# Performance work log

Hardware: AMD Instinct MI355X
Metric: run time of the kernel (lower is better)

Reference implementation:

```python
import jax, jax.numpy as jnp
import numpy as np

DILATED = (1, 2, 3)
NUM_PROTOS = 100
PROTO_SIZE = 4
ENC_SIZE = 1600
NUM_CLASSES = 2
B, L = 64, 256

# num_filters split exactly as in torch: floor(P/len) each, first gets remainder
_nf = [NUM_PROTOS // len(DILATED)] * len(DILATED)
_nf[0] += NUM_PROTOS % len(DILATED)
NUM_FILTERS = tuple(_nf)  # (34, 33, 33)


def setup_inputs() -> dict:
    key = jax.random.key(0)
    k1, k2, k3 = jax.random.split(key, 3)
    embedding = jax.random.normal(k1, (B, L, ENC_SIZE), dtype=jnp.float32)
    # nn.init.uniform_ default is U[0,1)
    protolayer = jax.random.uniform(k2, (NUM_PROTOS, ENC_SIZE, PROTO_SIZE), dtype=jnp.float32)
    fc_w = jax.random.normal(k3, (NUM_CLASSES, NUM_PROTOS), dtype=jnp.float32) * 0.1
    return {"embedding": embedding, "protolayer": protolayer, "fc_w": fc_w}


def _l2_convolution(x_bel, protolayer):
    # x_bel: [B, L, E] -> [B, E, L] for NCH conv layout
    x = jnp.transpose(x_bel, (0, 2, 1))
    # sliding-window sum of x^2 computed ONCE per dilation (shared across protos,
    # mathematically identical to conv1d with all-ones weight)
    s = jnp.sum(x * x, axis=1)  # [B, L]
    p2_sum = jnp.sum(protolayer * protolayer, axis=(1, 2))  # [P]
    distances = []
    j = 0
    Lx = x.shape[2]
    for d, n in zip(DILATED, NUM_FILTERS):
        L_out = Lx - (PROTO_SIZE - 1) * d
        # windowed sum over K=PROTO_SIZE taps with dilation d: [B, L_out]
        x2_patch = sum(s[:, k * d:k * d + L_out] for k in range(PROTO_SIZE))
        # dilated cross-correlation x * p : [B, n, L_out]
        xp = jax.lax.conv_general_dilated(
            x, protolayer[j:j + n],
            window_strides=(1,), padding='VALID', rhs_dilation=(d,),
            dimension_numbers=('NCH', 'OIH', 'NCH'))
        dist = jnp.sqrt(jnp.abs(x2_patch[:, None, :] - 2.0 * xp
                                + p2_sum[j:j + n][None, :, None]))
        distances.append(dist)
        j += n
    return distances


def reference(embedding, protolayer, fc_w):
    distances = _l2_convolution(embedding, protolayer)
    prototype_distances = jnp.concatenate(
        [jnp.min(d, axis=2) for d in distances], axis=1)  # [B, P]
    class_out = prototype_distances @ fc_w.T  # [B, num_classes]
    return (prototype_distances, distances[0], distances[1], distances[2], class_out)
```

## Files before the change

kernel.cpp:

```cpp
#include <hip/hip_runtime.h>

#define B_   64
#define L_   256
#define E_   1600
#define P_   100
#define KP   4
#define N0 34
#define N1 33
#define N2 33
#define LOUT0 253
#define LOUT1 250
#define LOUT2 247
#define OFF_PD 0
#define OFF_D0 6400
#define OFF_D1 (OFF_D0 + B_*N0*LOUT0)
#define OFF_D2 (OFF_D1 + B_*N1*LOUT1)
#define OFF_CO (OFF_D2 + B_*N2*LOUT2)

#define WS_ABF  0ull
#define WS_BT   52428800ull
#define WS_S    (WS_BT + 1280000ull)
#define WS_P2   (WS_S + 65536ull)
#define WS_NEED (WS_P2 + 512ull)

#define TMF  96
#define BKB  128
#define BOFF2 12288

typedef float f32x4 __attribute__((ext_vector_type(4)));
typedef unsigned short ushort8v __attribute__((ext_vector_type(8)));
typedef __bf16 bf16x8 __attribute__((ext_vector_type(8)));
typedef _Float16 f16;

__device__ __forceinline__ unsigned short bf16rne(float f) {
    unsigned u = __float_as_uint(f);
    u += 0x7FFFu + ((u >> 16) & 1u);
    return (unsigned short)(u >> 16);
}

typedef __attribute__((address_space(3))) void lds_void_t;
typedef __attribute__((address_space(1))) void glb_void_t;

__device__ __forceinline__ void gload16(const void* g, void* l) {
    __builtin_amdgcn_global_load_lds((const glb_void_t*)g, (lds_void_t*)l, 16, 0, 0);
}


__global__ __launch_bounds__(256) void proto_prep_fast(
        const float* __restrict__ emb, const float* __restrict__ proto,
        char* __restrict__ ws, float* __restrict__ out) {
    int q = blockIdx.x;
    int wave = threadIdx.x >> 6, lane = threadIdx.x & 63;
    if (q < 4096) {
        int row = q * 4 + wave;
        const float4* r = (const float4*)(emb + (size_t)row * E_);
        unsigned short* dst = (unsigned short*)(ws + WS_ABF + (size_t)row * (E_*2));
        float acc = 0.f;
        #pragma unroll
        for (int it = 0; it < 6; ++it) {
            int e4 = it * 64 + lane;
            float4 v = r[e4];
            acc += v.x*v.x + v.y*v.y + v.z*v.z + v.w*v.w;
            ushort4 bv = make_ushort4(bf16rne(v.x), bf16rne(v.y),
                                      bf16rne(v.z), bf16rne(v.w));
            *(ushort4*)(dst + e4 * 4) = bv;
        }
        if (lane < 16) {
            int e4 = 384 + lane;
            float4 v = r[e4];
            acc += v.x*v.x + v.y*v.y + v.z*v.z + v.w*v.w;
            ushort4 bv = make_ushort4(bf16rne(v.x), bf16rne(v.y),
                                      bf16rne(v.z), bf16rne(v.w));
            *(ushort4*)(dst + e4 * 4) = bv;
        }
        #pragma unroll
        for (int off = 32; off; off >>= 1) acc += __shfl_down(acc, off);
        if (lane == 0) ((float*)(ws + WS_S))[row] = acc;
    } else if (q < 4121) {
        int p = (q - 4096) * 4 + wave;
        if (p < P_) {
            const float4* r = (const float4*)(proto + (size_t)p * (E_ * KP));
            unsigned short* bt = (unsigned short*)(ws + WS_BT);
            float acc = 0.f;
            #pragma unroll
            for (int it = 0; it < 25; ++it) {
                int e = it * 64 + lane;
                float4 v = r[e];
                acc += v.x*v.x + v.y*v.y + v.z*v.z + v.w*v.w;
                bt[(size_t)(4*p + 0) * E_ + e] = bf16rne(v.x);
                bt[(size_t)(4*p + 1) * E_ + e] = bf16rne(v.y);
                bt[(size_t)(4*p + 2) * E_ + e] = bf16rne(v.z);
                bt[(size_t)(4*p + 3) * E_ + e] = bf16rne(v.w);
            }
            #pragma unroll
            for (int off = 32; off; off >>= 1) acc += __shfl_down(acc, off);
            if (lane == 0) ((float*)(ws + WS_P2))[p] = acc;
        }
    } else {
        for (int i = threadIdx.x; i < B_ * P_; i += 256)
            out[OFF_PD + i] = __uint_as_float(0x7F800000u);
    }
}

__global__ __launch_bounds__(384, 6) void proto_main_fast(
        const char* __restrict__ ws, float* __restrict__ out) {

    __shared__ __align__(16) char smem[22528];

    int bx   = blockIdx.x;
    int lb   = (bx & 7) * 120 + (bx >> 3);
    int b     = lb / 15;
    int inner = lb % 15;
    int m     = inner / 5;
    int n_blk = inner % 5;
    int r0    = (m == 0) ? 0 : (m == 1 ? 87 : 160);
    int l_lo  = m * 87;
    int pbase = n_blk * 20;

    const char* Ag = ws + WS_ABF + (size_t)(b * L_ + r0) * (E_ * 2);
    const char* Bg = ws + WS_BT  + (size_t)(pbase * 4) * (E_ * 2);

    int tid   = threadIdx.x;
    int lane  = tid & 63;
    int wave  = tid >> 6;
    int mrow  = lane & 15;
    int jq    = lane >> 4;
    int lrow8 = lane >> 3;
    int jst   = lane & 7;

    f32x4 acc[5] = {};

    for (int c = 0; c < 25; ++c) {
        int eoff = c * BKB;
        for (int t = wave; t < 22; t += 6) {
            if (t < 12) {
                int rowl = t * 8 + lrow8;
                int j = jst ^ (rowl & 7);
                gload16(Ag + (size_t)rowl * (E_*2) + eoff + j * 16,
                        smem + t * 1024);
            } else {
                int rowl = (t - 12) * 8 + lrow8;
                int j = jst ^ (rowl & 7);
                gload16(Bg + (size_t)rowl * (E_*2) + eoff + j * 16,
                        smem + BOFF2 + (t - 12) * 1024);
            }
        }
        __syncthreads();

        #pragma unroll
        for (int ks = 0; ks < 2; ++ks) {
            int rowA = wave * 16 + mrow;
            ushort8v af = *(const ushort8v*)(smem + rowA * 128
                            + (((ks << 2) + jq) ^ (rowA & 7)) * 16);
            ushort8v bfv[5];
            #pragma unroll
            for (int ni = 0; ni < 5; ++ni) {
                int rowB = ni * 16 + mrow;
                bfv[ni] = *(const ushort8v*)(smem + BOFF2 + rowB * 128
                            + (((ks << 2) + jq) ^ (rowB & 7)) * 16);
            }
            #pragma unroll
            for (int ni = 0; ni < 5; ++ni)
                acc[ni] = __builtin_amdgcn_mfma_f32_16x16x32_bf16(
                    __builtin_bit_cast(bf16x8, af),
                    __builtin_bit_cast(bf16x8, bfv[ni]),
                    acc[ni], 0, 0, 0);
        }
        __syncthreads();
    }

    f16*      Yh     = (f16*)smem;
    float*    slds   = (float*)(smem + 15552);
    float*    p2lds  = slds + TMF;
    unsigned* minlds = (unsigned*)(p2lds + 20);

    {
        int colq = lane & 15;
        int rowq = (lane >> 4) * 4;
        int row = wave * 16 + rowq;
        #pragma unroll
        for (int ni = 0; ni < 5; ++ni) {
            int col = ni * 16 + colq;
            #pragma unroll
            for (int r = 0; r < 4; ++r)
                Yh[(row + r) * 81 + col] = (f16)acc[ni][r];
        }
    }
    if (tid < TMF) slds[tid] = ((const float*)(ws + WS_S))[b * L_ + r0 + tid];
    if (tid < 20) {
        p2lds[tid] = ((const float*)(ws + WS_P2))[pbase + tid];
        minlds[tid] = 0x7F800000u;
    }
    __syncthreads();

    for (int idx = tid; idx < 20 * 87; idx += 384) {
        int pl  = idx / 87;
        int lof = idx % 87;
        int p = pbase + pl;
        int d, Lout, nseg, pseg; size_t segbase;
        if (p < 34)      { d = 1; Lout = LOUT0; segbase = OFF_D0; pseg = p;      nseg = N0; }
        else if (p < 67) { d = 2; Lout = LOUT1; segbase = OFF_D1; pseg = p - 34; nseg = N1; }
        else             { d = 3; Lout = LOUT2; segbase = OFF_D2; pseg = p - 67; nseg = N2; }
        int l = l_lo + lof;
        if (l < Lout) {
            int rl = l - r0;
            int c0 = pl * 4;
            float xp = (float)Yh[rl * 81 + c0]
                     + (float)Yh[(rl + d) * 81 + c0 + 1]
                     + (float)Yh[(rl + 2*d) * 81 + c0 + 2]
                     + (float)Yh[(rl + 3*d) * 81 + c0 + 3];
            float x2 = slds[rl] + slds[rl + d] + slds[rl + 2*d] + slds[rl + 3*d];
            float dist = sqrtf(fabsf(x2 - 2.f * xp + p2lds[pl]));
            out[segbase + ((size_t)b * nseg + pseg) * Lout + l] = dist;
            atomicMin(&minlds[pl], __float_as_uint(dist));
        }
    }
    __syncthreads();
    if (tid < 20)
        atomicMin((unsigned*)out + OFF_PD + b * P_ + pbase + tid, minlds[tid]);
}

#define TM   144
#define ASTR 40
#define YSTR 81

__global__ __launch_bounds__(256) void proto_prep_kernel(
        const float* __restrict__ emb, const float* __restrict__ proto,
        float* __restrict__ ws_s, float* __restrict__ ws_p2,
        float* __restrict__ out) {
    int q = blockIdx.x;
    int wave = threadIdx.x >> 6, lane = threadIdx.x & 63;
    if (q < 4096) {
        int row = q * 4 + wave;
        const float4* r = (const float4*)(emb + (size_t)row * E_);
        float acc = 0.f;
        #pragma unroll
        for (int it = 0; it < 7; ++it) {
            int e4 = it * 64 + lane;
            if (e4 < 400) {
                float4 v = r[e4];
                acc += v.x*v.x + v.y*v.y + v.z*v.z + v.w*v.w;
            }
        }
        #pragma unroll
        for (int off = 32; off; off >>= 1) acc += __shfl_down(acc, off);
        if (lane == 0) ws_s[row] = acc;
    } else if (q < 4121) {
        int p = (q - 4096) * 4 + wave;
        if (p < P_) {
            const float4* r = (const float4*)(proto + (size_t)p * (E_ * KP));
            float acc = 0.f;
            #pragma unroll
            for (int it = 0; it < 25; ++it) {
                float4 v = r[it * 64 + lane];
                acc += v.x*v.x + v.y*v.y + v.z*v.z + v.w*v.w;
            }
            #pragma unroll
            for (int off = 32; off; off >>= 1) acc += __shfl_down(acc, off);
            if (lane == 0) ws_p2[p] = acc;
        }
    } else {
        for (int i = threadIdx.x; i < B_ * P_; i += 256)
            out[OFF_PD + i] = __uint_as_float(0x7F800000u);
    }
}

__global__ __launch_bounds__(192) void proto_main_kernel(
        const float* __restrict__ emb, const float* __restrict__ proto,
        const float* __restrict__ ws_s, const float* __restrict__ ws_p2,
        float* __restrict__ out) {

    __shared__ __align__(16) char smem[47392];
    unsigned short* Ald = (unsigned short*)smem;
    unsigned short* Bld = (unsigned short*)(smem + TM*ASTR*2);

    int bx = blockIdx.x;
    int n_blk = bx % 5;
    int m     = (bx / 5) & 1;
    int b     = bx / 10;
    int r0    = m ? 112 : 0;
    int pbase = n_blk * 20;

    const float* Abase = emb + ((size_t)(b * L_ + r0)) * E_;
    const float* Bbase = proto + (size_t)pbase * (E_ * KP);

    int tid  = threadIdx.x;
    int lane = tid & 63;
    int wave = tid >> 6;
    int mrow = lane & 15;
    int kq   = (lane >> 4) * 8;

    f32x4 acc[3][5] = {};

    for (int c = 0; c < E_ / 32; ++c) {
        int e0 = c * 32;
        #pragma unroll
        for (int i = 0; i < 6; ++i) {
            int idx = tid + i * 192;
            int row = idx >> 3;
            int e4  = idx & 7;
            float4 v = *(const float4*)(Abase + (size_t)row * E_ + e0 + e4 * 4);
            ushort4 bv = make_ushort4(bf16rne(v.x), bf16rne(v.y),
                                      bf16rne(v.z), bf16rne(v.w));
            *(ushort4*)&Ald[row * ASTR + e4 * 4] = bv;
        }
        for (int idx = tid; idx < 640; idx += 192) {
            int pl = idx >> 5;
            int el = idx & 31;
            float4 v = *(const float4*)(Bbase + (size_t)pl * (E_ * KP)
                                        + (size_t)(e0 + el) * KP);
            Bld[(4*pl + 0) * ASTR + el] = bf16rne(v.x);
            Bld[(4*pl + 1) * ASTR + el] = bf16rne(v.y);
            Bld[(4*pl + 2) * ASTR + el] = bf16rne(v.z);
            Bld[(4*pl + 3) * ASTR + el] = bf16rne(v.w);
        }
        __syncthreads();

        ushort8v af[3], bfr[5];
        #pragma unroll
        for (int mi = 0; mi < 3; ++mi)
            af[mi] = *(const ushort8v*)&Ald[(wave*48 + mi*16 + mrow) * ASTR + kq];
        #pragma unroll
        for (int ni = 0; ni < 5; ++ni)
            bfr[ni] = *(const ushort8v*)&Bld[(ni*16 + mrow) * ASTR + kq];
        #pragma unroll
        for (int mi = 0; mi < 3; ++mi)
            #pragma unroll
            for (int ni = 0; ni < 5; ++ni)
                acc[mi][ni] = __builtin_amdgcn_mfma_f32_16x16x32_bf16(
                    __builtin_bit_cast(bf16x8, af[mi]),
                    __builtin_bit_cast(bf16x8, bfr[ni]),
                    acc[mi][ni], 0, 0, 0);
        __syncthreads();
    }

    float*    Ylds   = (float*)smem;
    float*    slds   = (float*)(smem + TM * YSTR * 4);
    float*    p2lds  = slds + TM;
    unsigned* minlds = (unsigned*)(p2lds + 20);

    {
        int colq = lane & 15;
        int rowq = (lane >> 4) * 4;
        #pragma unroll
        for (int mi = 0; mi < 3; ++mi) {
            int row = wave * 48 + mi * 16 + rowq;
            #pragma unroll
            for (int ni = 0; ni < 5; ++ni) {
                int col = ni * 16 + colq;
                #pragma unroll
                for (int r = 0; r < 4; ++r)
                    Ylds[(row + r) * YSTR + col] = acc[mi][ni][r];
            }
        }
    }
    if (tid < TM) slds[tid] = ws_s[b * L_ + r0 + tid];
    if (tid < 20) { p2lds[tid] = ws_p2[pbase + tid]; minlds[tid] = 0x7F800000u; }
    __syncthreads();

    int l_lo = m * 128;
    for (int idx = tid; idx < 20 * 128; idx += 192) {
        int pl  = idx >> 7;
        int lof = idx & 127;
        int p = pbase + pl;
        int d, Lout, nseg, pseg; size_t segbase;
        if (p < 34)      { d = 1; Lout = LOUT0; segbase = OFF_D0; pseg = p;      nseg = N0; }
        else if (p < 67) { d = 2; Lout = LOUT1; segbase = OFF_D1; pseg = p - 34; nseg = N1; }
        else             { d = 3; Lout = LOUT2; segbase = OFF_D2; pseg = p - 67; nseg = N2; }
        int l = l_lo + lof;
        if (l < Lout) {
            int rl = l - r0;
            int c0 = pl * 4;
            float xp = Ylds[rl * YSTR + c0]
                     + Ylds[(rl + d) * YSTR + c0 + 1]
                     + Ylds[(rl + 2*d) * YSTR + c0 + 2]
                     + Ylds[(rl + 3*d) * YSTR + c0 + 3];
            float x2 = slds[rl] + slds[rl + d] + slds[rl + 2*d] + slds[rl + 3*d];
            float dist = sqrtf(fabsf(x2 - 2.f * xp + p2lds[pl]));
            out[segbase + ((size_t)b * nseg + pseg) * Lout + l] = dist;
            atomicMin(&minlds[pl], __float_as_uint(dist));
        }
    }
    __syncthreads();
    if (tid < 20)
        atomicMin((unsigned*)out + OFF_PD + b * P_ + pbase + tid, minlds[tid]);
}

__global__ __launch_bounds__(128) void proto_fc_kernel(
        const float* __restrict__ fc_w, float* __restrict__ out) {
    int t = threadIdx.x;
    int b = t >> 1, c = t & 1;
    const float* pd = out + OFF_PD + b * P_;
    const float* w  = fc_w + c * P_;
    float s = 0.f;
    #pragma unroll 4
    for (int p = 0; p < P_; ++p) s += pd[p] * w[p];
    out[OFF_CO + b * 2 + c] = s;
}

extern "C" void kernel_launch(void* const* d_in, const int* in_sizes, int n_in,
                              void* d_out, int out_size, void* d_ws, size_t ws_size,
                              hipStream_t stream) {
    const float* emb   = (const float*)d_in[0];
    const float* proto = (const float*)d_in[1];
    const float* fc_w  = (const float*)d_in[2];
    float* out  = (float*)d_out;

    if (ws_size >= WS_NEED) {
        char* ws = (char*)d_ws;
        proto_prep_fast<<<4122, 256, 0, stream>>>(emb, proto, ws, out);
        proto_main_fast<<<960, 384, 0, stream>>>(ws, out);
    } else {
        float* ws_s  = (float*)d_ws;
        float* ws_p2 = ws_s + B_ * L_;
        proto_prep_kernel<<<4122, 256, 0, stream>>>(emb, proto, ws_s, ws_p2, out);
        proto_main_kernel<<<640, 192, 0, stream>>>(emb, proto, ws_s, ws_p2, out);
    }
    proto_fc_kernel<<<1, 128, 0, stream>>>(fc_w, out);
}
```

Measured before the change: 211.2 us.

## Double-buffer LDS tiles in main GEMM loop and fuse fc into last block

```diff
diff --git a/kernel.cpp b/kernel.cpp
--- a/kernel.cpp
+++ b/kernel.cpp
@@ -21,11 +21,13 @@
 #define WS_BT   52428800ull
 #define WS_S    (WS_BT + 1280000ull)
 #define WS_P2   (WS_S + 65536ull)
-#define WS_NEED (WS_P2 + 512ull)
+#define WS_CNT  (WS_P2 + 512ull)
+#define WS_NEED (WS_CNT + 256ull)
 
 #define TMF  96
 #define BKB  128
 #define BOFF2 12288
+#define BUFSZ 22528
 
 typedef float f32x4 __attribute__((ext_vector_type(4)));
 typedef unsigned short ushort8v __attribute__((ext_vector_type(8)));
@@ -99,13 +101,17 @@
     } else {
         for (int i = threadIdx.x; i < B_ * P_; i += 256)
             out[OFF_PD + i] = __uint_as_float(0x7F800000u);
-    }
-}
-
-__global__ __launch_bounds__(384, 6) void proto_main_fast(
-        const char* __restrict__ ws, float* __restrict__ out) {
-
-    __shared__ __align__(16) char smem[22528];
+        if (threadIdx.x < 64)
+            ((unsigned*)(ws + WS_CNT))[threadIdx.x] = 0u;
+    }
+}
+
+__global__ __launch_bounds__(384, 4) void proto_main_fast(
+        char* __restrict__ ws, const float* __restrict__ fc_w,
+        float* __restrict__ out) {
+
+    __shared__ __align__(16) char smem[2 * BUFSZ];
+    __shared__ int lastf;
 
     int bx   = blockIdx.x;
     int lb   = (bx & 7) * 120 + (bx >> 3);
@@ -130,33 +136,49 @@
 
     f32x4 acc[5] = {};
 
+    for (int t = wave; t < 22; t += 6) {
+        if (t < 12) {
+            int rowl = t * 8 + lrow8;
+            int j = jst ^ (rowl & 7);
+            gload16(Ag + (size_t)rowl * (E_*2) + j * 16, smem + t * 1024);
+        } else {
+            int rowl = (t - 12) * 8 + lrow8;
+            int j = jst ^ (rowl & 7);
+            gload16(Bg + (size_t)rowl * (E_*2) + j * 16,
+                    smem + BOFF2 + (t - 12) * 1024);
+        }
+    }
+    __syncthreads();
+
     for (int c = 0; c < 25; ++c) {
-        int eoff = c * BKB;
-        for (int t = wave; t < 22; t += 6) {
-            if (t < 12) {
-                int rowl = t * 8 + lrow8;
-                int j = jst ^ (rowl & 7);
-                gload16(Ag + (size_t)rowl * (E_*2) + eoff + j * 16,
-                        smem + t * 1024);
-            } else {
-                int rowl = (t - 12) * 8 + lrow8;
-                int j = jst ^ (rowl & 7);
-                gload16(Bg + (size_t)rowl * (E_*2) + eoff + j * 16,
-                        smem + BOFF2 + (t - 12) * 1024);
-            }
-        }
-        __syncthreads();
-
+        const char* cbuf = smem + (c & 1) * BUFSZ;
+        if (c < 24) {
+            char* nbuf = smem + ((c + 1) & 1) * BUFSZ;
+            int eoff = (c + 1) * BKB;
+            for (int t = wave; t < 22; t += 6) {
+                if (t < 12) {
+                    int rowl = t * 8 + lrow8;
+                    int j = jst ^ (rowl & 7);
+                    gload16(Ag + (size_t)rowl * (E_*2) + eoff + j * 16,
+                            nbuf + t * 1024);
+                } else {
+                    int rowl = (t - 12) * 8 + lrow8;
+                    int j = jst ^ (rowl & 7);
+                    gload16(Bg + (size_t)rowl * (E_*2) + eoff + j * 16,
+                            nbuf + BOFF2 + (t - 12) * 1024);
+                }
+            }
+        }
         #pragma unroll
         for (int ks = 0; ks < 2; ++ks) {
             int rowA = wave * 16 + mrow;
-            ushort8v af = *(const ushort8v*)(smem + rowA * 128
+            ushort8v af = *(const ushort8v*)(cbuf + rowA * 128
                             + (((ks << 2) + jq) ^ (rowA & 7)) * 16);
             ushort8v bfv[5];
             #pragma unroll
             for (int ni = 0; ni < 5; ++ni) {
                 int rowB = ni * 16 + mrow;
-                bfv[ni] = *(const ushort8v*)(smem + BOFF2 + rowB * 128
+                bfv[ni] = *(const ushort8v*)(cbuf + BOFF2 + rowB * 128
                             + (((ks << 2) + jq) ^ (rowB & 7)) * 16);
             }
             #pragma unroll
@@ -218,6 +240,28 @@
     __syncthreads();
     if (tid < 20)
         atomicMin((unsigned*)out + OFF_PD + b * P_ + pbase + tid, minlds[tid]);
+
+    __syncthreads();
+    if (tid == 0) {
+        __threadfence();
+        unsigned prev = atomicAdd((unsigned*)(ws + WS_CNT) + b, 1u);
+        lastf = (prev == 14u);
+    }
+    __syncthreads();
+    if (lastf && tid < 128) {
+        int cls = tid >> 6;
+        int ln  = tid & 63;
+        float s = 0.f;
+        for (int p = ln; p < P_; p += 64) {
+            float v = __hip_atomic_load(
+                (const float*)out + OFF_PD + b * P_ + p,
+                __ATOMIC_RELAXED, __HIP_MEMORY_SCOPE_AGENT);
+            s += v * fc_w[cls * P_ + p];
+        }
+        #pragma unroll
+        for (int off = 32; off; off >>= 1) s += __shfl_down(s, off);
+        if (ln == 0) out[OFF_CO + b * 2 + cls] = s;
+    }
 }
 
 #define TM   144
@@ -409,12 +453,12 @@
     if (ws_size >= WS_NEED) {
         char* ws = (char*)d_ws;
         proto_prep_fast<<<4122, 256, 0, stream>>>(emb, proto, ws, out);
-        proto_main_fast<<<960, 384, 0, stream>>>(ws, out);
+        proto_main_fast<<<960, 384, 0, stream>>>(ws, fc_w, out);
     } else {
         float* ws_s  = (float*)d_ws;
         float* ws_p2 = ws_s + B_ * L_;
         proto_prep_kernel<<<4122, 256, 0, stream>>>(emb, proto, ws_s, ws_p2, out);
         proto_main_kernel<<<640, 192, 0, stream>>>(emb, proto, ws_s, ws_p2, out);
-    }
-    proto_fc_kernel<<<1, 128, 0, stream>>>(fc_w, out);
-}
+        proto_fc_kernel<<<1, 128, 0, stream>>>(fc_w, out);
+    }
+}
```

Result: slower. 240.2 us (+13.7%).
